# Performance work log

Measured on AMD Instinct MI355X. Metric: run time of the kernel, lower is better.

## Reference

```python
import jax, jax.numpy as jnp
import numpy as np

NUM_HEADS = 16
QMAX = 127.0  # int8 symmetric

def fake_quant(x):
    # symmetric per-tensor int8 quantize -> dequantize (models Quantize/QLinear numerics)
    scale = jnp.maximum(jnp.max(jnp.abs(x)) / QMAX, 1e-8)
    q = jnp.clip(jnp.round(x / scale), -QMAX, QMAX) * scale
    # straight-through estimator (no-op in fwd-only, keeps fwd/bwd code identical)
    return x + jax.lax.stop_gradient(q - x)

def setup_inputs() -> dict:
    key = jax.random.key(0)
    ks = jax.random.split(key, 5)
    B, T, C = 2, 2048, 1024
    return {
        "x": jax.random.normal(ks[0], (B, T, C), jnp.float32),
        "Wqkv": jax.random.normal(ks[1], (3 * C, C), jnp.float32) * (C ** -0.5),
        "bqkv": jax.random.normal(ks[2], (3 * C,), jnp.float32) * 0.01,
        "Wproj": jax.random.normal(ks[3], (C, C), jnp.float32) * (C ** -0.5),
        "bproj": jax.random.normal(ks[4], (C,), jnp.float32) * 0.01,
    }

def reference(x, Wqkv, bqkv, Wproj, bproj):
    B, T, C = x.shape
    H = NUM_HEADS
    D = C // H
    scale = D ** -0.5
    # quantized input + quantized-weight linear (dequantized to fp32 afterwards)
    xq = fake_quant(x)
    qkv = xq @ fake_quant(Wqkv).T + bqkv                      # [B, T, 3C]
    qkv = qkv.reshape(B, T, 3, H, D).transpose(2, 0, 3, 1, 4)  # [3, B, H, T, D]
    q, k, v = qkv[0], qkv[1], qkv[2]
    scores = jnp.einsum("bhqd,bhkd->bhqk", q, k) * scale       # [B, H, T, T]
    causal = jnp.triu(jnp.full((T, T), -jnp.inf, jnp.float32), k=1)
    attn = jax.nn.softmax(scores + causal, axis=-1)
    # dropout: eval mode -> identity
    out = jnp.einsum("bhqk,bhkd->bhqd", attn, v)               # [B, H, T, D]
    out = out.transpose(0, 2, 1, 3).reshape(B, T, C)
    outq = fake_quant(out)
    return outq @ fake_quant(Wproj).T + bproj
```

## Files before the change

kernel.cpp:

```cpp
#include <hip/hip_runtime.h>
#include <hip/hip_bf16.h>
#include <stdint.h>

typedef __bf16 bf16_t;
typedef bf16_t bf16x4 __attribute__((ext_vector_type(4)));
typedef bf16_t bf16x8 __attribute__((ext_vector_type(8)));
typedef short s16x4 __attribute__((ext_vector_type(4)));
typedef int i32x4 __attribute__((ext_vector_type(4)));
typedef float f32x4 __attribute__((ext_vector_type(4)));
typedef unsigned int u32;
typedef u32 u32x4 __attribute__((ext_vector_type(4)));
typedef u32 u32x2 __attribute__((ext_vector_type(2)));

#define QMAXF 127.0f
#define CSC 0.18033688f

__device__ __forceinline__ void gl16(const void* g, void* l) {
  __builtin_amdgcn_global_load_lds(
      (__attribute__((address_space(1))) void*)(g),
      (__attribute__((address_space(3))) void*)(l), 16, 0, 0);
}

__global__ __launch_bounds__(256) void amax3_kernel(const float* __restrict__ p0, int n0,
                                                    const float* __restrict__ p1, int n1,
                                                    const float* __restrict__ p2, int n2,
                                                    float* __restrict__ dst) {
  const float* p; int n; float* d; int b0, nb;
  if (blockIdx.x < 512)      { p = p0; n = n0; d = dst + 0; b0 = 0;   nb = 512; }
  else if (blockIdx.x < 768) { p = p1; n = n1; d = dst + 1; b0 = 512; nb = 256; }
  else                       { p = p2; n = n2; d = dst + 2; b0 = 768; nb = 128; }
  const int n4 = n >> 2;
  const int stride = nb * 256;
  float m = 0.f;
  for (int i = (blockIdx.x - b0) * 256 + threadIdx.x; i < n4; i += stride) {
    const f32x4 v = ((const f32x4*)p)[i];
    m = fmaxf(m, fmaxf(fmaxf(fabsf(v[0]), fabsf(v[1])), fmaxf(fabsf(v[2]), fabsf(v[3]))));
  }
#pragma unroll
  for (int dd = 1; dd < 64; dd <<= 1) m = fmaxf(m, __shfl_xor(m, dd));
  __shared__ float sm[4];
  if ((threadIdx.x & 63) == 0) sm[threadIdx.x >> 6] = m;
  __syncthreads();
  if (threadIdx.x == 0) {
    float mm = fmaxf(fmaxf(sm[0], sm[1]), fmaxf(sm[2], sm[3]));
    atomicMax((int*)d, __float_as_int(mm));
  }
}

__device__ __forceinline__ void quant_body(const float* __restrict__ p, int n,
                                           const float* __restrict__ amax,
                                           int8_t* __restrict__ q, int bid, int nb) {
  const float s = fmaxf(amax[0] / QMAXF, 1e-8f);
  const int n4 = n >> 2;
  const int stride = nb * 256;
  for (int i = bid * 256 + (int)threadIdx.x; i < n4; i += stride) {
    const f32x4 v = ((const f32x4*)p)[i];
    int r[4];
#pragma unroll
    for (int j = 0; j < 4; j++) {
      float t = rintf(v[j] / s);
      t = fminf(127.f, fmaxf(-127.f, t));
      r[j] = (int)t;
    }
    ((uint32_t*)q)[i] = (uint32_t)(r[0] & 0xff) | ((uint32_t)(r[1] & 0xff) << 8) |
                        ((uint32_t)(r[2] & 0xff) << 16) | ((uint32_t)(r[3] & 0xff) << 24);
  }
}

__global__ __launch_bounds__(256) void quant3_kernel(const float* __restrict__ p0, int n0,
                                                     const float* __restrict__ p1, int n1,
                                                     const float* __restrict__ p2, int n2,
                                                     const float* __restrict__ amax,
                                                     int8_t* __restrict__ q0,
                                                     int8_t* __restrict__ q1,
                                                     int8_t* __restrict__ q2) {
  if (blockIdx.x < 512)      quant_body(p0, n0, amax + 0, q0, blockIdx.x, 512);
  else if (blockIdx.x < 768) quant_body(p1, n1, amax + 1, q1, blockIdx.x - 512, 256);
  else                       quant_body(p2, n2, amax + 2, q2, blockIdx.x - 768, 128);
}

__global__ __launch_bounds__(256) void quant_bf16_kernel(const u32* __restrict__ p,
                                                         int n,
                                                         const float* __restrict__ amax,
                                                         int8_t* __restrict__ q) {
  const float s = fmaxf(amax[0] / QMAXF, 1e-8f);
  const int n8 = n >> 3;
  const int stride = gridDim.x * blockDim.x;
  for (int i = blockIdx.x * blockDim.x + (int)threadIdx.x; i < n8; i += stride) {
    const u32x4 v = ((const u32x4*)p)[i];
    int r[8];
#pragma unroll
    for (int k = 0; k < 4; k++) {
      const float lo = __uint_as_float(v[k] << 16);
      const float hi = __uint_as_float(v[k] & 0xffff0000u);
      float t0 = fminf(127.f, fmaxf(-127.f, rintf(lo / s)));
      float t1 = fminf(127.f, fmaxf(-127.f, rintf(hi / s)));
      r[2 * k] = (int)t0; r[2 * k + 1] = (int)t1;
    }
    u32x2 o;
    o[0] = (u32)(r[0] & 0xff) | ((u32)(r[1] & 0xff) << 8) |
           ((u32)(r[2] & 0xff) << 16) | ((u32)(r[3] & 0xff) << 24);
    o[1] = (u32)(r[4] & 0xff) | ((u32)(r[5] & 0xff) << 8) |
           ((u32)(r[6] & 0xff) << 16) | ((u32)(r[7] & 0xff) << 24);
    ((u32x2*)q)[i] = o;
  }
}

template <int MODE>
__global__ __launch_bounds__(256) void gemm_i8_kernel(
    const int8_t* __restrict__ A, const int8_t* __restrict__ Bw,
    const float* __restrict__ amaxA, const float* __restrict__ amaxB,
    const float* __restrict__ bias,
    bf16_t* __restrict__ qkv_out, bf16_t* __restrict__ vt_out, float* __restrict__ f_out) {
  constexpr int K = 1024;
  __shared__ int8_t As[2][8192];
  __shared__ int8_t Bs[2][8192];
  const int tid = threadIdx.x;
  const int lane = tid & 63;
  const int w = tid >> 6, wr = w >> 1, wc = w & 1;
  const int l15 = lane & 15, lg = lane >> 4;
  const int bm = blockIdx.y * 128, bn = blockIdx.x * 128;

  const int sr = tid >> 2;
  const int sc = (tid & 3) * 16;
  const int8_t* gA = A + (size_t)(bm + sr) * K + sc;
  const int8_t* gB = Bw + (size_t)(bn + sr) * K + sc;

  auto stage = [&](int k0, int buf) {
    gl16(gA + k0, As[buf] + tid * 16);
    gl16(gA + 64 * K + k0, As[buf] + 4096 + tid * 16);
    gl16(gB + k0, Bs[buf] + tid * 16);
    gl16(gB + 64 * K + k0, Bs[buf] + 4096 + tid * 16);
  };

  i32x4 acc[4][4] = {};

  stage(0, 0);
  __syncthreads();
  for (int ks = 0; ks < K / 64; ks++) {
    const int buf = ks & 1;
    if (ks + 1 < K / 64) stage((ks + 1) * 64, buf ^ 1);
    i32x4 aF[4], bF[4];
#pragma unroll
    for (int m = 0; m < 4; m++)
      aF[m] = *(const i32x4*)(As[buf] + (wr * 64 + m * 16 + l15) * 64 + lg * 16);
#pragma unroll
    for (int n = 0; n < 4; n++)
      bF[n] = *(const i32x4*)(Bs[buf] + (wc * 64 + n * 16 + l15) * 64 + lg * 16);
#pragma unroll
    for (int m = 0; m < 4; m++)
#pragma unroll
      for (int n = 0; n < 4; n++)
        acc[m][n] = __builtin_amdgcn_mfma_i32_16x16x64_i8(aF[m], bF[n], acc[m][n], 0, 0, 0);
    __syncthreads();
  }

  const float sA = fmaxf(amaxA[0] / QMAXF, 1e-8f);
  const float sB = fmaxf(amaxB[0] / QMAXF, 1e-8f);
  const float s = sA * sB;

#pragma unroll
  for (int m = 0; m < 4; m++) {
#pragma unroll
    for (int n = 0; n < 4; n++) {
      const int c = bn + wc * 64 + n * 16 + l15;
      const float bs = bias[c];
      const int r0 = bm + wr * 64 + m * 16 + lg * 4;
      float vv[4];
#pragma unroll
      for (int reg = 0; reg < 4; reg++) vv[reg] = (float)acc[m][n][reg] * s + bs;
      if (MODE == 0) {
        const int which = c >> 10, hd = c & 1023;
        if (which < 2) {
          const float qs = (which == 0) ? CSC : 1.0f;
#pragma unroll
          for (int reg = 0; reg < 4; reg++) {
            const int r = r0 + reg;
            const int b = r >> 11, t = r & 2047;
            qkv_out[(size_t)which * (32u * 2048 * 64) +
                    (size_t)((((b << 4) + (hd >> 6)) * 2048 + t) << 6) + (hd & 63)] =
                (bf16_t)(vv[reg] * qs);
          }
        } else {
          const int b = r0 >> 11, t0 = r0 & 2047;
          const int h = hd >> 6, d = hd & 63;
          bf16x4 pk;
#pragma unroll
          for (int reg = 0; reg < 4; reg++) pk[reg] = (bf16_t)vv[reg];
          *(bf16x4*)(vt_out + ((size_t)((b << 4) + h) * 64 + d) * 2048 + t0) = pk;
        }
      } else {
#pragma unroll
        for (int reg = 0; reg < 4; reg++) f_out[(size_t)(r0 + reg) * 1024 + c] = vv[reg];
      }
    }
  }
}

__global__ __launch_bounds__(256, 2) void attn_kernel(
    const bf16_t* __restrict__ Qg, const bf16_t* __restrict__ Kg, const bf16_t* __restrict__ VTg,
    bf16_t* __restrict__ Out, float* __restrict__ amax_out) {
  const int bh = blockIdx.x;
  const int pairi = blockIdx.y;
  const int tid = threadIdx.x, lane = tid & 63, w = tid >> 6;
  const int l15 = lane & 15, lg = lane >> 4;
  const int b = bh >> 4, h = bh & 15;

  const bf16_t* Qp = Qg + (size_t)bh * 2048 * 64;
  const char* Kbase = (const char*)(Kg + (size_t)bh * 2048 * 64);
  const char* Vbase = (const char*)(VTg + (size_t)bh * 64 * 2048);

  __shared__ __align__(16) bf16_t Kb[3][4096];
  __shared__ __align__(16) bf16_t Vb[3][4096];

  auto stage = [&](int kv0, int buf) {
#pragma unroll
    for (int i = 0; i < 4; i++) {
      const int o = ((w & 1) * 4 + i) * 1024 + lane * 16;
      const int row = o >> 7;
      const int sbc = (o & 127) ^ ((row & 7) << 4);
      if (w < 2)
        gl16(Kbase + (size_t)(kv0 + row) * 128 + sbc, (char*)Kb[buf] + o);
      else
        gl16(Vbase + (size_t)row * 4096 + (size_t)kv0 * 2 + sbc, (char*)Vb[buf] + o);
    }
  };

  float am = 0.f;
  for (int half = 0; half < 2; ++half) {
    const int S = half ? (31 - pairi) : pairi;
    const int qb = S * 64 + w * 16;
    const int nt = S + 1;
    const int qrow = qb + l15;

    bf16x8 qf[2];
#pragma unroll
    for (int ks = 0; ks < 2; ks++)
      qf[ks] = *(const bf16x8*)(Qp + (size_t)(qb + l15) * 64 + ks * 32 + lg * 8);

    f32x4 acc[4] = {};
    float lsum = 0.f;

    stage(0, 0);
    if (nt > 1) stage(64, 1);

    for (int it = 0; it < nt; ++it) {
      const int sl = it % 3;
      const int kv0 = it * 64;

      if (it + 1 < nt) { asm volatile("s_waitcnt vmcnt(4)" ::: "memory"); }
      else             { asm volatile("s_waitcnt vmcnt(0)" ::: "memory"); }
      __builtin_amdgcn_sched_barrier(0);
      __builtin_amdgcn_s_barrier();
      __builtin_amdgcn_sched_barrier(0);

      bf16x8 kF[4][2];
#pragma unroll
      for (int rf = 0; rf < 4; rf++)
#pragma unroll
        for (int ks = 0; ks < 2; ks++) {
          const int row = rf * 16 + l15;
          kF[rf][ks] = *(const bf16x8*)((const char*)Kb[sl] + row * 128 +
                                        ((ks * 64 + lg * 16) ^ ((row & 7) << 4)));
        }
      s16x4 vB[4][4];
#pragma unroll
      for (int cf = 0; cf < 4; cf++)
#pragma unroll
        for (int rf = 0; rf < 4; rf++) {
          const int row = cf * 16 + l15;
          vB[cf][rf] = *(const s16x4*)((const char*)Vb[sl] + row * 128 +
                                       ((rf * 32 + lg * 8) ^ ((row & 7) << 4)));
        }
      if (it + 2 < nt) stage(kv0 + 128, (it + 2) % 3);
      asm volatile("s_waitcnt lgkmcnt(0)" ::: "memory");
      __builtin_amdgcn_sched_barrier(0);

      f32x4 sfT[4] = {};
      __builtin_amdgcn_s_setprio(1);
#pragma unroll
      for (int rf = 0; rf < 4; rf++)
#pragma unroll
        for (int ks = 0; ks < 2; ks++)
          sfT[rf] = __builtin_amdgcn_mfma_f32_16x16x32_bf16(kF[rf][ks], qf[ks], sfT[rf], 0, 0, 0);
      __builtin_amdgcn_s_setprio(0);

      const bool need_mask = (it == nt - 1);
      float p[16];
#pragma unroll
      for (int rf = 0; rf < 4; rf++)
#pragma unroll
        for (int reg = 0; reg < 4; reg++) {
          float v = sfT[rf][reg];
          if (need_mask && (kv0 + rf * 16 + lg * 4 + reg > qrow)) v = -1e30f;
          p[rf * 4 + reg] = __builtin_amdgcn_exp2f(v);
        }
      float s01 = (p[0] + p[1]) + (p[2] + p[3]);
      float s23 = (p[4] + p[5]) + (p[6] + p[7]);
      float s45 = (p[8] + p[9]) + (p[10] + p[11]);
      float s67 = (p[12] + p[13]) + (p[14] + p[15]);
      lsum += (s01 + s23) + (s45 + s67);

      s16x4 pa[4];
#pragma unroll
      for (int rf = 0; rf < 4; rf++) {
        bf16x4 t;
#pragma unroll
        for (int reg = 0; reg < 4; reg++) t[reg] = (bf16_t)p[rf * 4 + reg];
        pa[rf] = __builtin_bit_cast(s16x4, t);
      }
      __builtin_amdgcn_s_setprio(1);
#pragma unroll
      for (int cf = 0; cf < 4; cf++)
#pragma unroll
        for (int rf = 0; rf < 4; rf++)
          acc[cf] = __builtin_amdgcn_mfma_f32_16x16x16bf16_1k(pa[rf], vB[cf][rf], acc[cf], 0, 0, 0);
      __builtin_amdgcn_s_setprio(0);
    }

    lsum += __shfl_xor(lsum, 16);
    lsum += __shfl_xor(lsum, 32);
    const float inv = 1.0f / lsum;
    float iq[4];
#pragma unroll
    for (int reg = 0; reg < 4; reg++) iq[reg] = __shfl(inv, lg * 4 + reg);
#pragma unroll
    for (int cf = 0; cf < 4; cf++)
#pragma unroll
      for (int reg = 0; reg < 4; reg++) {
        const float v = acc[cf][reg] * iq[reg];
        am = fmaxf(am, fabsf(v));
        const int t = qb + lg * 4 + reg;
        Out[(size_t)(b * 2048 + t) * 1024 + h * 64 + cf * 16 + l15] = (bf16_t)v;
      }

    __syncthreads();
  }

#pragma unroll
  for (int dd = 1; dd < 64; dd <<= 1) am = fmaxf(am, __shfl_xor(am, dd));
  if (lane == 0) atomicMax((int*)amax_out, __float_as_int(am));
}

extern "C" void kernel_launch(void* const* d_in, const int* in_sizes, int n_in,
                              void* d_out, int out_size, void* d_ws, size_t ws_size,
                              hipStream_t stream) {
  const float* x = (const float*)d_in[0];
  const float* Wqkv = (const float*)d_in[1];
  const float* bqkv = (const float*)d_in[2];
  const float* Wproj = (const float*)d_in[3];
  const float* bproj = (const float*)d_in[4];
  float* out = (float*)d_out;

  char* ws = (char*)d_ws;
  float* amax = (float*)ws;
  int8_t* xq = (int8_t*)(ws + 256);
  int8_t* wqq = xq + (size_t)4096 * 1024;
  int8_t* wpq = wqq + (size_t)3072 * 1024;
  bf16_t* qkv = (bf16_t*)(ws + 8388864);
  bf16_t* Q = qkv;
  bf16_t* Kk = qkv + (size_t)32 * 2048 * 64;
  bf16_t* VT = qkv + (size_t)2 * 32 * 2048 * 64;
  bf16_t* aout = (bf16_t*)(ws + 33554688);
  int8_t* outq = (int8_t*)(ws + 50331904);

  hipMemsetAsync(amax, 0, 16, stream);
  amax3_kernel<<<896, 256, 0, stream>>>(x, 4194304, Wqkv, 3145728, Wproj, 1048576, amax);
  quant3_kernel<<<896, 256, 0, stream>>>(x, 4194304, Wqkv, 3145728, Wproj, 1048576, amax,
                                         xq, wqq, wpq);
  gemm_i8_kernel<0><<<dim3(24, 32), 256, 0, stream>>>(xq, wqq, amax + 0, amax + 1, bqkv,
                                                      qkv, VT, nullptr);
  attn_kernel<<<dim3(32, 16), 256, 0, stream>>>(Q, Kk, VT, aout, amax + 3);
  quant_bf16_kernel<<<512, 256, 0, stream>>>((const u32*)aout, 4194304, amax + 3, outq);
  gemm_i8_kernel<1><<<dim3(8, 32), 256, 0, stream>>>(outq, wpq, amax + 3, amax + 2, bproj,
                                                     nullptr, nullptr, out);
}
```

Baseline: 126.1 us.

## Use 128-key KV tiles with double buffering in attention kernel

Doubles the key/value tile from 64 to 128 keys, halving the number of inner-loop iterations and the barriers per query block. The three-deep LDS ring with explicit vmcnt waits becomes a two-buffer scheme: the next tile is prefetched at the start of each iteration and a __syncthreads closes it. The aim is to amortise per-iteration barrier and bookkeeping cost over more MFMA work. In exchange it needs more registers for the K/V fragments, more LDS (64KB), and hides load latency less. Up to 64 keys on the last causal tile are masked but still computed.

```diff
diff --git a/kernel.cpp b/kernel.cpp
--- a/kernel.cpp
+++ b/kernel.cpp
@@ -210,19 +210,23 @@
   const char* Kbase = (const char*)(Kg + (size_t)bh * 2048 * 64);
   const char* Vbase = (const char*)(VTg + (size_t)bh * 64 * 2048);
 
-  __shared__ __align__(16) bf16_t Kb[3][4096];
-  __shared__ __align__(16) bf16_t Vb[3][4096];
+  __shared__ __align__(16) bf16_t Kb[2][128 * 64];
+  __shared__ __align__(16) bf16_t Vb[2][64 * 128];
 
   auto stage = [&](int kv0, int buf) {
 #pragma unroll
-    for (int i = 0; i < 4; i++) {
-      const int o = ((w & 1) * 4 + i) * 1024 + lane * 16;
-      const int row = o >> 7;
-      const int sbc = (o & 127) ^ ((row & 7) << 4);
-      if (w < 2)
+    for (int i = 0; i < 8; i++) {
+      if (w < 2) {
+        const int o = (w * 8 + i) * 1024 + lane * 16;
+        const int row = o >> 7;
+        const int sbc = (o & 127) ^ ((row & 7) << 4);
         gl16(Kbase + (size_t)(kv0 + row) * 128 + sbc, (char*)Kb[buf] + o);
-      else
+      } else {
+        const int o = ((w - 2) * 8 + i) * 1024 + lane * 16;
+        const int row = o >> 8;
+        const int sbc = (o & 255) ^ ((row & 15) << 4);
         gl16(Vbase + (size_t)row * 4096 + (size_t)kv0 * 2 + sbc, (char*)Vb[buf] + o);
+      }
     }
   };
 
@@ -230,7 +234,7 @@
   for (int half = 0; half < 2; ++half) {
     const int S = half ? (31 - pairi) : pairi;
     const int qb = S * 64 + w * 16;
-    const int nt = S + 1;
+    const int nt = (S >> 1) + 1;
     const int qrow = qb + l15;
 
     bf16x8 qf[2];
@@ -242,68 +246,63 @@
     float lsum = 0.f;
 
     stage(0, 0);
-    if (nt > 1) stage(64, 1);
+    __syncthreads();
 
     for (int it = 0; it < nt; ++it) {
-      const int sl = it % 3;
-      const int kv0 = it * 64;
-
-      if (it + 1 < nt) { asm volatile("s_waitcnt vmcnt(4)" ::: "memory"); }
-      else             { asm volatile("s_waitcnt vmcnt(0)" ::: "memory"); }
-      __builtin_amdgcn_sched_barrier(0);
-      __builtin_amdgcn_s_barrier();
-      __builtin_amdgcn_sched_barrier(0);
-
-      bf16x8 kF[4][2];
-#pragma unroll
-      for (int rf = 0; rf < 4; rf++)
+      const int buf = it & 1;
+      const int kv0 = it * 128;
+      if (it + 1 < nt) stage(kv0 + 128, buf ^ 1);
+
+      bf16x8 kF[8][2];
+#pragma unroll
+      for (int rf = 0; rf < 8; rf++)
 #pragma unroll
         for (int ks = 0; ks < 2; ks++) {
           const int row = rf * 16 + l15;
-          kF[rf][ks] = *(const bf16x8*)((const char*)Kb[sl] + row * 128 +
+          kF[rf][ks] = *(const bf16x8*)((const char*)Kb[buf] + row * 128 +
                                         ((ks * 64 + lg * 16) ^ ((row & 7) << 4)));
         }
-      s16x4 vB[4][4];
+      s16x4 vB[4][8];
 #pragma unroll
       for (int cf = 0; cf < 4; cf++)
 #pragma unroll
-        for (int rf = 0; rf < 4; rf++) {
+        for (int rf = 0; rf < 8; rf++) {
           const int row = cf * 16 + l15;
-          vB[cf][rf] = *(const s16x4*)((const char*)Vb[sl] + row * 128 +
-                                       ((rf * 32 + lg * 8) ^ ((row & 7) << 4)));
+          vB[cf][rf] = *(const s16x4*)((const char*)Vb[buf] + row * 256 +
+                                       ((rf * 32 + lg * 8) ^ ((row & 15) << 4)));
         }
-      if (it + 2 < nt) stage(kv0 + 128, (it + 2) % 3);
       asm volatile("s_waitcnt lgkmcnt(0)" ::: "memory");
       __builtin_amdgcn_sched_barrier(0);
 
-      f32x4 sfT[4] = {};
+      f32x4 sfT[8] = {};
       __builtin_amdgcn_s_setprio(1);
 #pragma unroll
-      for (int rf = 0; rf < 4; rf++)
+      for (int rf = 0; rf < 8; rf++)
 #pragma unroll
         for (int ks = 0; ks < 2; ks++)
           sfT[rf] = __builtin_amdgcn_mfma_f32_16x16x32_bf16(kF[rf][ks], qf[ks], sfT[rf], 0, 0, 0);
       __builtin_amdgcn_s_setprio(0);
 
       const bool need_mask = (it == nt - 1);
-      float p[16];
-#pragma unroll
-      for (int rf = 0; rf < 4; rf++)
+      float p[32];
+#pragma unroll
+      for (int rf = 0; rf < 8; rf++)
 #pragma unroll
         for (int reg = 0; reg < 4; reg++) {
           float v = sfT[rf][reg];
           if (need_mask && (kv0 + rf * 16 + lg * 4 + reg > qrow)) v = -1e30f;
           p[rf * 4 + reg] = __builtin_amdgcn_exp2f(v);
         }
-      float s01 = (p[0] + p[1]) + (p[2] + p[3]);
-      float s23 = (p[4] + p[5]) + (p[6] + p[7]);
-      float s45 = (p[8] + p[9]) + (p[10] + p[11]);
-      float s67 = (p[12] + p[13]) + (p[14] + p[15]);
-      lsum += (s01 + s23) + (s45 + s67);
-
-      s16x4 pa[4];
-#pragma unroll
-      for (int rf = 0; rf < 4; rf++) {
+      float t0 = 0.f, t1 = 0.f, t2 = 0.f, t3 = 0.f;
+#pragma unroll
+      for (int i = 0; i < 8; i++) {
+        t0 += p[i]; t1 += p[8 + i]; t2 += p[16 + i]; t3 += p[24 + i];
+      }
+      lsum += (t0 + t1) + (t2 + t3);
+
+      s16x4 pa[8];
+#pragma unroll
+      for (int rf = 0; rf < 8; rf++) {
         bf16x4 t;
 #pragma unroll
         for (int reg = 0; reg < 4; reg++) t[reg] = (bf16_t)p[rf * 4 + reg];
@@ -313,9 +312,11 @@
 #pragma unroll
       for (int cf = 0; cf < 4; cf++)
 #pragma unroll
-        for (int rf = 0; rf < 4; rf++)
+        for (int rf = 0; rf < 8; rf++)
           acc[cf] = __builtin_amdgcn_mfma_f32_16x16x16bf16_1k(pa[rf], vB[cf][rf], acc[cf], 0, 0, 0);
       __builtin_amdgcn_s_setprio(0);
+
+      __syncthreads();
     }
 
     lsum += __shfl_xor(lsum, 16);
```

Result: slower. 132.1 us (+4.7%).

## Process paired causal query blocks in one KV sweep sharing K/V tiles

Applied to the files above, without the earlier changes.

Instead of running two sequential passes over KV for the short (pairi) and long (31-pairi) query blocks, the kernel now walks the KV range once and computes both query blocks against each staged K/V tile. The short block participates only while it <= SA. This halves the global-to-LDS K/V traffic for the overlapping prefix and removes the second pipeline prologue and the inter-pass syncthreads. In exchange it raises register pressure, with two accumulator sets and two Q fragments live, which could lower occupancy or cause spills.

```diff
diff --git a/kernel.cpp b/kernel.cpp
--- a/kernel.cpp
+++ b/kernel.cpp
@@ -226,80 +226,91 @@
     }
   };
 
-  float am = 0.f;
-  for (int half = 0; half < 2; ++half) {
-    const int S = half ? (31 - pairi) : pairi;
-    const int qb = S * 64 + w * 16;
-    const int nt = S + 1;
-    const int qrow = qb + l15;
-
-    bf16x8 qf[2];
-#pragma unroll
-    for (int ks = 0; ks < 2; ks++)
-      qf[ks] = *(const bf16x8*)(Qp + (size_t)(qb + l15) * 64 + ks * 32 + lg * 8);
-
-    f32x4 acc[4] = {};
-    float lsum = 0.f;
-
-    stage(0, 0);
-    if (nt > 1) stage(64, 1);
-
-    for (int it = 0; it < nt; ++it) {
-      const int sl = it % 3;
-      const int kv0 = it * 64;
-
-      if (it + 1 < nt) { asm volatile("s_waitcnt vmcnt(4)" ::: "memory"); }
-      else             { asm volatile("s_waitcnt vmcnt(0)" ::: "memory"); }
-      __builtin_amdgcn_sched_barrier(0);
-      __builtin_amdgcn_s_barrier();
-      __builtin_amdgcn_sched_barrier(0);
-
-      bf16x8 kF[4][2];
+  const int SA = pairi;
+  const int SB = 31 - pairi;
+  const int nt = SB + 1;
+  const int qbA = SA * 64 + w * 16, qbB = SB * 64 + w * 16;
+  const int qrowA = qbA + l15, qrowB = qbB + l15;
+
+  bf16x8 qfA[2], qfB[2];
+#pragma unroll
+  for (int ks = 0; ks < 2; ks++) {
+    qfA[ks] = *(const bf16x8*)(Qp + (size_t)(qbA + l15) * 64 + ks * 32 + lg * 8);
+    qfB[ks] = *(const bf16x8*)(Qp + (size_t)(qbB + l15) * 64 + ks * 32 + lg * 8);
+  }
+
+  f32x4 accA[4] = {}, accB[4] = {};
+  float lsumA = 0.f, lsumB = 0.f;
+
+  stage(0, 0);
+  stage(64, 1);
+
+  for (int it = 0; it < nt; ++it) {
+    const int sl = it % 3;
+    const int kv0 = it * 64;
+
+    if (it + 1 < nt) { asm volatile("s_waitcnt vmcnt(4)" ::: "memory"); }
+    else             { asm volatile("s_waitcnt vmcnt(0)" ::: "memory"); }
+    __builtin_amdgcn_sched_barrier(0);
+    __builtin_amdgcn_s_barrier();
+    __builtin_amdgcn_sched_barrier(0);
+
+    bf16x8 kF[4][2];
+#pragma unroll
+    for (int rf = 0; rf < 4; rf++)
+#pragma unroll
+      for (int ks = 0; ks < 2; ks++) {
+        const int row = rf * 16 + l15;
+        kF[rf][ks] = *(const bf16x8*)((const char*)Kb[sl] + row * 128 +
+                                      ((ks * 64 + lg * 16) ^ ((row & 7) << 4)));
+      }
+    s16x4 vB[4][4];
+#pragma unroll
+    for (int cf = 0; cf < 4; cf++)
+#pragma unroll
+      for (int rf = 0; rf < 4; rf++) {
+        const int row = cf * 16 + l15;
+        vB[cf][rf] = *(const s16x4*)((const char*)Vb[sl] + row * 128 +
+                                     ((rf * 32 + lg * 8) ^ ((row & 7) << 4)));
+      }
+    if (it + 2 < nt) stage(kv0 + 128, (it + 2) % 3);
+    asm volatile("s_waitcnt lgkmcnt(0)" ::: "memory");
+    __builtin_amdgcn_sched_barrier(0);
+
+    f32x4 sfB[4] = {};
+    __builtin_amdgcn_s_setprio(1);
+#pragma unroll
+    for (int rf = 0; rf < 4; rf++)
+#pragma unroll
+      for (int ks = 0; ks < 2; ks++)
+        sfB[rf] = __builtin_amdgcn_mfma_f32_16x16x32_bf16(kF[rf][ks], qfB[ks], sfB[rf], 0, 0, 0);
+    __builtin_amdgcn_s_setprio(0);
+
+    if (it <= SA) {
+      f32x4 sfA[4] = {};
+      __builtin_amdgcn_s_setprio(1);
 #pragma unroll
       for (int rf = 0; rf < 4; rf++)
 #pragma unroll
-        for (int ks = 0; ks < 2; ks++) {
-          const int row = rf * 16 + l15;
-          kF[rf][ks] = *(const bf16x8*)((const char*)Kb[sl] + row * 128 +
-                                        ((ks * 64 + lg * 16) ^ ((row & 7) << 4)));
-        }
-      s16x4 vB[4][4];
-#pragma unroll
-      for (int cf = 0; cf < 4; cf++)
-#pragma unroll
-        for (int rf = 0; rf < 4; rf++) {
-          const int row = cf * 16 + l15;
-          vB[cf][rf] = *(const s16x4*)((const char*)Vb[sl] + row * 128 +
-                                       ((rf * 32 + lg * 8) ^ ((row & 7) << 4)));
-        }
-      if (it + 2 < nt) stage(kv0 + 128, (it + 2) % 3);
-      asm volatile("s_waitcnt lgkmcnt(0)" ::: "memory");
-      __builtin_amdgcn_sched_barrier(0);
-
-      f32x4 sfT[4] = {};
-      __builtin_amdgcn_s_setprio(1);
+        for (int ks = 0; ks < 2; ks++)
+          sfA[rf] = __builtin_amdgcn_mfma_f32_16x16x32_bf16(kF[rf][ks], qfA[ks], sfA[rf], 0, 0, 0);
+      __builtin_amdgcn_s_setprio(0);
+
+      const bool maskA = (it == SA);
+      float p[16];
 #pragma unroll
       for (int rf = 0; rf < 4; rf++)
 #pragma unroll
-        for (int ks = 0; ks < 2; ks++)
-          sfT[rf] = __builtin_amdgcn_mfma_f32_16x16x32_bf16(kF[rf][ks], qf[ks], sfT[rf], 0, 0, 0);
-      __builtin_amdgcn_s_setprio(0);
-
-      const bool need_mask = (it == nt - 1);
-      float p[16];
-#pragma unroll
-      for (int rf = 0; rf < 4; rf++)
-#pragma unroll
         for (int reg = 0; reg < 4; reg++) {
-          float v = sfT[rf][reg];
-          if (need_mask && (kv0 + rf * 16 + lg * 4 + reg > qrow)) v = -1e30f;
+          float v = sfA[rf][reg];
+          if (maskA && (kv0 + rf * 16 + lg * 4 + reg > qrowA)) v = -1e30f;
           p[rf * 4 + reg] = __builtin_amdgcn_exp2f(v);
         }
       float s01 = (p[0] + p[1]) + (p[2] + p[3]);
       float s23 = (p[4] + p[5]) + (p[6] + p[7]);
       float s45 = (p[8] + p[9]) + (p[10] + p[11]);
       float s67 = (p[12] + p[13]) + (p[14] + p[15]);
-      lsum += (s01 + s23) + (s45 + s67);
+      lsumA += (s01 + s23) + (s45 + s67);
 
       s16x4 pa[4];
 #pragma unroll
@@ -314,13 +325,51 @@
       for (int cf = 0; cf < 4; cf++)
 #pragma unroll
         for (int rf = 0; rf < 4; rf++)
-          acc[cf] = __builtin_amdgcn_mfma_f32_16x16x16bf16_1k(pa[rf], vB[cf][rf], acc[cf], 0, 0, 0);
+          accA[cf] = __builtin_amdgcn_mfma_f32_16x16x16bf16_1k(pa[rf], vB[cf][rf], accA[cf], 0, 0, 0);
       __builtin_amdgcn_s_setprio(0);
     }
 
-    lsum += __shfl_xor(lsum, 16);
-    lsum += __shfl_xor(lsum, 32);
-    const float inv = 1.0f / lsum;
+    {
+      const bool maskB = (it == nt - 1);
+      float p[16];
+#pragma unroll
+      for (int rf = 0; rf < 4; rf++)
+#pragma unroll
+        for (int reg = 0; reg < 4; reg++) {
+          float v = sfB[rf][reg];
+          if (maskB && (kv0 + rf * 16 + lg * 4 + reg > qrowB)) v = -1e30f;
+          p[rf * 4 + reg] = __builtin_amdgcn_exp2f(v);
+        }
+      float s01 = (p[0] + p[1]) + (p[2] + p[3]);
+      float s23 = (p[4] + p[5]) + (p[6] + p[7]);
+      float s45 = (p[8] + p[9]) + (p[10] + p[11]);
+      float s67 = (p[12] + p[13]) + (p[14] + p[15]);
+      lsumB += (s01 + s23) + (s45 + s67);
+
+      s16x4 pa[4];
+#pragma unroll
+      for (int rf = 0; rf < 4; rf++) {
+        bf16x4 t;
+#pragma unroll
+        for (int reg = 0; reg < 4; reg++) t[reg] = (bf16_t)p[rf * 4 + reg];
+        pa[rf] = __builtin_bit_cast(s16x4, t);
+      }
+      __builtin_amdgcn_s_setprio(1);
+#pragma unroll
+      for (int cf = 0; cf < 4; cf++)
+#pragma unroll
+        for (int rf = 0; rf < 4; rf++)
+          accB[cf] = __builtin_amdgcn_mfma_f32_16x16x16bf16_1k(pa[rf], vB[cf][rf], accB[cf], 0, 0, 0);
+      __builtin_amdgcn_s_setprio(0);
+    }
+  }
+
+  float am = 0.f;
+  {
+    float ls = lsumA;
+    ls += __shfl_xor(ls, 16);
+    ls += __shfl_xor(ls, 32);
+    const float inv = 1.0f / ls;
     float iq[4];
 #pragma unroll
     for (int reg = 0; reg < 4; reg++) iq[reg] = __shfl(inv, lg * 4 + reg);
@@ -328,13 +377,29 @@
     for (int cf = 0; cf < 4; cf++)
 #pragma unroll
       for (int reg = 0; reg < 4; reg++) {
-        const float v = acc[cf][reg] * iq[reg];
+        const float v = accA[cf][reg] * iq[reg];
         am = fmaxf(am, fabsf(v));
-        const int t = qb + lg * 4 + reg;
+        const int t = qbA + lg * 4 + reg;
         Out[(size_t)(b * 2048 + t) * 1024 + h * 64 + cf * 16 + l15] = (bf16_t)v;
       }
-
-    __syncthreads();
+  }
+  {
+    float ls = lsumB;
+    ls += __shfl_xor(ls, 16);
+    ls += __shfl_xor(ls, 32);
+    const float inv = 1.0f / ls;
+    float iq[4];
+#pragma unroll
+    for (int reg = 0; reg < 4; reg++) iq[reg] = __shfl(inv, lg * 4 + reg);
+#pragma unroll
+    for (int cf = 0; cf < 4; cf++)
+#pragma unroll
+      for (int reg = 0; reg < 4; reg++) {
+        const float v = accB[cf][reg] * iq[reg];
+        am = fmaxf(am, fabsf(v));
+        const int t = qbB + lg * 4 + reg;
+        Out[(size_t)(b * 2048 + t) * 1024 + h * 64 + cf * 16 + l15] = (bf16_t)v;
+      }
   }
 
 #pragma unroll
```

Result: slower. 128.7 us (+2.0%).
